# Performance work log

Hardware: AMD Instinct MI355X
Metric: run time of the kernel (lower is better)

## Reference

```python
import jax, jax.numpy as jnp
import numpy as np

DIM = 1024
NUM_HEADS = 16
HEAD_DIM = DIM // NUM_HEADS  # 64
LATENT = 128
Q_RANK = 256
B, S = 4, 2048


def setup_inputs() -> dict:
    key = jax.random.key(0)
    ks = jax.random.split(key, 12)
    w = lambda k, shape: jax.random.normal(k, shape, dtype=jnp.float32) * 0.02
    x = jax.random.normal(ks[0], (B, S, DIM), dtype=jnp.float32)
    mask = jnp.tril(jnp.ones((S, S), dtype=jnp.int32))[None, None, :, :]  # causal [1,1,S,S]
    return {
        "x": x,
        "mask": mask,
        "w_kvc": w(ks[1], (DIM, LATENT)),   "b_kvc": jnp.zeros((LATENT,), jnp.float32),
        "w_kvu": w(ks[2], (LATENT, 2 * DIM)), "b_kvu": jnp.zeros((2 * DIM,), jnp.float32),
        "w_qc":  w(ks[3], (DIM, Q_RANK)),   "b_qc": jnp.zeros((Q_RANK,), jnp.float32),
        "w_qu":  w(ks[4], (Q_RANK, DIM)),   "b_qu": jnp.zeros((DIM,), jnp.float32),
        "w_o":   w(ks[5], (DIM, DIM)),      "b_o": jnp.zeros((DIM,), jnp.float32),
    }


def reference(x, mask, w_kvc, b_kvc, w_kvu, b_kvu, w_qc, b_qc, w_qu, b_qu, w_o, b_o):
    b, s, _ = x.shape
    # low-rank KV path
    kv_latent = x @ w_kvc + b_kvc                      # [B,S,latent]
    kv_up = kv_latent @ w_kvu + b_kvu                  # [B,S,2*dim]
    K, V = jnp.split(kv_up, 2, axis=-1)                # each [B,S,dim]
    # low-rank Q path
    Q = (x @ w_qc + b_qc) @ w_qu + b_qu                # [B,S,dim]

    def split_heads(t):  # [B,S,dim] -> [B,H,S,hd]
        return t.reshape(b, s, NUM_HEADS, HEAD_DIM).transpose(0, 2, 1, 3)

    Qh, Kh, Vh = split_heads(Q), split_heads(K), split_heads(V)
    scores = jnp.einsum("bhsd,bhtd->bhst", Qh, Kh) / np.sqrt(HEAD_DIM).astype(np.float32)
    scores = jnp.where(mask == 0, jnp.float32(-1e9), scores)
    attn = jax.nn.softmax(scores, axis=-1)
    ctx = jnp.einsum("bhst,bhtd->bhsd", attn, Vh)      # [B,H,S,hd]
    ctx = ctx.transpose(0, 2, 1, 3).reshape(b, s, DIM)
    return ctx @ w_o + b_o
```

## Files before the change

### kernel.cpp

```cpp
#include <hip/hip_runtime.h>

typedef __attribute__((ext_vector_type(8))) short short8;
typedef __attribute__((ext_vector_type(4))) float f32x4;

#define DIM 1024
#define NH 16
#define HD 64
#define LAT 128
#define QR 256
#define NCAT (LAT + QR)
#define BB 4
#define SS 2048
#define BS (BB * SS)

#define SCALE_LOG2E 0.18033688011112042f

__device__ __forceinline__ unsigned short f2b(float f) {
  unsigned int u = __builtin_bit_cast(unsigned int, f);
  u += 0x7FFFu + ((u >> 16) & 1u);
  return (unsigned short)(u >> 16);
}
__device__ __forceinline__ float b2f(unsigned short h) {
  unsigned int u = ((unsigned int)h) << 16;
  return __builtin_bit_cast(float, u);
}
__device__ __forceinline__ unsigned int pack_bf16_pair(float f0, float f1) {
  unsigned int u0 = __builtin_bit_cast(unsigned int, f0) + 0x8000u;
  unsigned int u1 = __builtin_bit_cast(unsigned int, f1) + 0x8000u;
  return __builtin_amdgcn_perm(u1, u0, 0x07060302u);
}
__device__ __forceinline__ void gll16(const unsigned short* g, unsigned short* l) {
  __builtin_amdgcn_global_load_lds(
      (const __attribute__((address_space(1))) unsigned int*)g,
      (__attribute__((address_space(3))) unsigned int*)l, 16, 0, 0);
}

__global__ __launch_bounds__(256) void cvt_x(const float* __restrict__ in,
                                             unsigned short* __restrict__ out, int n4) {
  int i = blockIdx.x * 256 + threadIdx.x;
  if (i >= n4) return;
  f32x4 v = ((const f32x4*)in)[i];
  ushort4 o;
  o.x = f2b(v[0]); o.y = f2b(v[1]); o.z = f2b(v[2]); o.w = f2b(v[3]);
  ((ushort4*)out)[i] = o;
}

__global__ __launch_bounds__(256) void prep_weights(
    const float* __restrict__ w_kvc, const float* __restrict__ w_qc,
    const float* __restrict__ w_kvu, const float* __restrict__ w_qu,
    const float* __restrict__ w_o, const float* __restrict__ b_kvc,
    const float* __restrict__ b_qc, unsigned short* __restrict__ wcatT,
    unsigned short* __restrict__ wkvuT, unsigned short* __restrict__ wquT,
    unsigned short* __restrict__ woT, float* __restrict__ bias_cat) {
  __shared__ unsigned short T[64 * 72];
  const int id = blockIdx.x;
  const int tid = threadIdx.x;
  if (id >= 480) {
    if (tid < LAT) bias_cat[tid] = b_kvc[tid];
    else bias_cat[tid] = b_qc[tid - LAT];
    if (tid < 128) bias_cat[tid + 256] = b_qc[tid + 128];
    return;
  }
  const float* in; unsigned short* out; int K, N, tile;
  if (id < 32)       { in = w_kvc; out = wcatT;                       K = DIM; N = LAT;     tile = id; }
  else if (id < 96)  { in = w_qc;  out = wcatT + (size_t)LAT * DIM;   K = DIM; N = QR;      tile = id - 32; }
  else if (id < 160) { in = w_kvu; out = wkvuT;                       K = LAT; N = 2 * DIM; tile = id - 96; }
  else if (id < 224) { in = w_qu;  out = wquT;                        K = QR;  N = DIM;     tile = id - 160; }
  else               { in = w_o;   out = woT;                         K = DIM; N = DIM;     tile = id - 224; }
  const int ktiles = K >> 6;
  const int k0 = (tile % ktiles) * 64, n0 = (tile / ktiles) * 64;
  {
    const int r = tid >> 2, cq = (tid & 3) * 16;
#pragma unroll
    for (int j = 0; j < 4; ++j) {
      f32x4 v = *(const f32x4*)(in + (size_t)(k0 + r) * N + n0 + cq + j * 4);
      ushort4 o;
      o.x = f2b(v[0]); o.y = f2b(v[1]); o.z = f2b(v[2]); o.w = f2b(v[3]);
      *(ushort4*)(T + r * 72 + cq + j * 4) = o;
    }
  }
  __syncthreads();
#pragma unroll
  for (int s = 0; s < 2; ++s) {
    int idx = tid + s * 256;
    int nr = idx >> 3, kg = (idx & 7) * 8;
    short8 o;
#pragma unroll
    for (int i = 0; i < 8; i++) o[i] = T[(kg + i) * 72 + nr];
    *(short8*)(out + (size_t)(n0 + nr) * K + k0 + kg) = o;
  }
}

__global__ __launch_bounds__(256, 4) void gemm_lds(const unsigned short* __restrict__ A,
                                                   const unsigned short* __restrict__ WT,
                                                   const float* __restrict__ bias,
                                                   float* __restrict__ outF,
                                                   unsigned short* __restrict__ outB,
                                                   unsigned short* __restrict__ vtOut,
                                                   int N, int K, int lda, int ldout,
                                                   float scale, int nblk) {
  __shared__ unsigned short gsm[17408];
  const int tid = threadIdx.x;
  const int wave = tid >> 6, lane = tid & 63;
  const int ln = lane & 15, quad = lane >> 4;
  const int chunk = nblk >> 3;
  const int sw = (blockIdx.x & 7) * chunk + (blockIdx.x >> 3);
  const int nwx = N >> 7;
  const int bx = sw % nwx, by = sw / nwx;
  const int m0 = by * 128, n0 = bx * 128;
  const int wm = (wave >> 1) * 64, wn = (wave & 1) * 64;

  const int srow = wave * 32 + (lane >> 2);
  const int scol = (lane & 3) * 8;
  const unsigned short* Ag = A + (size_t)(m0 + srow) * lda + scol;
  const unsigned short* Bg = WT + (size_t)(n0 + srow) * K + scol;

  f32x4 acc[4][4];
#pragma unroll
  for (int i = 0; i < 4; i++)
#pragma unroll
    for (int j = 0; j < 4; j++) acc[i][j] = (f32x4){0.f, 0.f, 0.f, 0.f};

#define STAGE(buf, kk)                                                        \
  {                                                                           \
    unsigned short* Al = gsm + (buf) * 4096 + wave * 1024;                    \
    unsigned short* Bl = gsm + 8192 + (buf) * 4096 + wave * 1024;             \
    gll16(Ag + (kk), Al);                                                     \
    gll16(Ag + (size_t)16 * lda + (kk), Al + 512);                            \
    gll16(Bg + (kk), Bl);                                                     \
    gll16(Bg + (size_t)16 * K + (kk), Bl + 512);                              \
  }

  STAGE(0, 0);
  __syncthreads();
  const int T = K >> 5;
  int cur = 0;
  for (int t = 0; t < T; ++t) {
    if (t + 1 < T) STAGE(cur ^ 1, (t + 1) * 32);
    const unsigned short* Ab = gsm + cur * 4096;
    const unsigned short* Bb = gsm + 8192 + cur * 4096;
    short8 af[4], bf[4];
#pragma unroll
    for (int i = 0; i < 4; i++) {
      af[i] = *(const short8*)(Ab + (wm + i * 16 + ln) * 32 + quad * 8);
      bf[i] = *(const short8*)(Bb + (wn + i * 16 + ln) * 32 + quad * 8);
    }
#pragma unroll
    for (int mi = 0; mi < 4; mi++)
#pragma unroll
      for (int ni = 0; ni < 4; ni++)
        acc[mi][ni] =
            __builtin_amdgcn_mfma_f32_16x16x32_bf16(af[mi], bf[ni], acc[mi][ni], 0, 0, 0);
    __syncthreads();
    cur ^= 1;
  }
#undef STAGE

  if (vtOut && n0 >= DIM) {
#pragma unroll
    for (int mi = 0; mi < 4; mi++) {
      const int s = wm + mi * 16 + quad * 4;
#pragma unroll
      for (int ni = 0; ni < 4; ni++) {
        const int d = wn + ni * 16 + ln;
        const float bv = bias[n0 + d];
#pragma unroll
        for (int r = 0; r < 4; r++)
          gsm[d * 136 + s + r] = f2b(acc[mi][ni][r] + bv);
      }
    }
    __syncthreads();
    const int d0 = n0 - DIM, bb = m0 >> 11, s0l = m0 & (SS - 1);
#pragma unroll
    for (int t = 0; t < 8; ++t) {
      int idx = tid + t * 256;
      int dr = idx >> 4, cs = (idx & 15) * 8;
      short8 v = *(const short8*)(gsm + dr * 136 + cs);
      *(short8*)(vtOut + (size_t)(bb * DIM + d0 + dr) * SS + s0l + cs) = v;
    }
    return;
  }

#pragma unroll
  for (int mi = 0; mi < 4; mi++) {
    const int row = m0 + wm + mi * 16 + quad * 4;
#pragma unroll
    for (int ni = 0; ni < 4; ni++) {
      const int col = n0 + wn + ni * 16 + ln;
      const float bv = bias[col];
#pragma unroll
      for (int r = 0; r < 4; r++) {
        float v = (acc[mi][ni][r] + bv) * scale;
        size_t o = (size_t)(row + r) * ldout + col;
        if (outF) outF[o] = v;
        if (outB) outB[o] = f2b(v);
      }
    }
  }
}

__global__ __launch_bounds__(256, 4) void attn_mfma(const unsigned short* __restrict__ Qb,
                                                    const unsigned short* __restrict__ KVb,
                                                    const unsigned short* __restrict__ VTb,
                                                    unsigned short* __restrict__ ctxB) {
  __shared__ unsigned short smem[12288];
  unsigned short* Ks = smem;
  unsigned short* Vts = smem + 4096;
  unsigned short* Ps = smem + 8192;
  const int tid = threadIdx.x;
  const int wave = tid >> 6, lane = tid & 63;
  const int ln = lane & 15, quad = lane >> 4;
  const int hw = blockIdx.x;
  const int xcd = hw & 7, slot = hw >> 3;
  const int grp = xcd * 8 + (slot >> 4);
  const int pair = slot & 15;
  const int h = grp & 15, b = grp >> 4;
  const int tA = pair, tB = 31 - pair;
  const int s0A = tA * 64, s0B = tB * 64;
  const int ktmaxB = tB;
  const int qminA = s0A + wave * 16, qmaxA = qminA + 15;
  const int qminB = s0B + wave * 16, qmaxB = qminB + 15;

  short8 qfA[2], qfB[2];
  {
    const unsigned short* qa =
        Qb + (size_t)(b * SS + s0A + wave * 16 + ln) * DIM + h * HD + quad * 8;
    qfA[0] = *(const short8*)qa;
    qfA[1] = *(const short8*)(qa + 32);
    const unsigned short* qb2 =
        Qb + (size_t)(b * SS + s0B + wave * 16 + ln) * DIM + h * HD + quad * 8;
    qfB[0] = *(const short8*)qb2;
    qfB[1] = *(const short8*)(qb2 + 32);
  }

  f32x4 ocA[4], ocB[4];
  float lpA = 0.f, lpB = 0.f;
#pragma unroll
  for (int i = 0; i < 4; i++) {
    ocA[i] = (f32x4){0.f, 0.f, 0.f, 0.f};
    ocB[i] = (f32x4){0.f, 0.f, 0.f, 0.f};
  }

  unsigned short* Pw = Ps + wave * (16 * 64);
  const int swz = (ln & 7) << 3;

  const int srow = tid >> 3, sc8 = (tid & 7) * 8;
  const int ssc = sc8 ^ ((srow & 7) << 3);

  const unsigned short* kptr =
      KVb + (size_t)(b * SS + srow) * (2 * DIM) + h * HD + sc8;
  const unsigned short* vptr = VTb + (size_t)(b * DIM + h * HD + srow) * SS + sc8;
  const size_t kstep = (size_t)64 * 2 * DIM;
  const size_t krow32 = (size_t)32 * 2 * DIM;
  const size_t vrow32 = (size_t)32 * SS;

  short8 kreg0 = *(const short8*)kptr;
  short8 kreg1 = *(const short8*)(kptr + krow32);
  short8 vreg0 = *(const short8*)vptr;
  short8 vreg1 = *(const short8*)(vptr + vrow32);

  for (int kt = 0; kt <= ktmaxB; ++kt) {
    __syncthreads();
    *(short8*)(Ks + srow * 64 + ssc) = kreg0;
    *(short8*)(Ks + (srow + 32) * 64 + ssc) = kreg1;
    *(short8*)(Vts + srow * 64 + ssc) = vreg0;
    *(short8*)(Vts + (srow + 32) * 64 + ssc) = vreg1;
    __syncthreads();
    if (kt < ktmaxB) {
      kptr += kstep; vptr += 64;
      kreg0 = *(const short8*)kptr;
      kreg1 = *(const short8*)(kptr + krow32);
      vreg0 = *(const short8*)vptr;
      vreg1 = *(const short8*)(vptr + vrow32);
    }

    const int k0g = kt * 64;

    auto stream = [&](const short8* qf, f32x4* oc, float& lp, const int qminw,
                      const int qmaxw) {
      if (k0g > qmaxw) return;
      const bool needmask = (k0g + 63 > qminw);

      f32x4 sacc[4];
#pragma unroll
      for (int nt = 0; nt < 4; nt++) sacc[nt] = (f32x4){0.f, 0.f, 0.f, 0.f};
      __builtin_amdgcn_s_setprio(1);
#pragma unroll
      for (int kc = 0; kc < 2; kc++) {
        const int rc = (kc * 32 + quad * 8) ^ swz;
#pragma unroll
        for (int nt = 0; nt < 4; nt++) {
          if (k0g + nt * 16 > qmaxw) continue;
          short8 kfrag = *(const short8*)(Ks + (nt * 16 + ln) * 64 + rc);
          sacc[nt] =
              __builtin_amdgcn_mfma_f32_16x16x32_bf16(kfrag, qf[kc], sacc[nt], 0, 0, 0);
        }
      }
      __builtin_amdgcn_s_setprio(0);

      const int qg = qminw + ln;
      float lt = 0.f;
      if (!needmask) {
#pragma unroll
        for (int nt = 0; nt < 4; nt++) {
          float p0 = __builtin_exp2f(sacc[nt][0]);
          float p1 = __builtin_exp2f(sacc[nt][1]);
          float p2 = __builtin_exp2f(sacc[nt][2]);
          float p3 = __builtin_exp2f(sacc[nt][3]);
          uint2 pw;
          pw.x = pack_bf16_pair(p0, p1);
          pw.y = pack_bf16_pair(p2, p3);
          *(uint2*)(Pw + ln * 64 + ((nt * 16 + quad * 4) ^ swz)) = pw;
          lt += (p0 + p1) + (p2 + p3);
        }
      } else {
#pragma unroll
        for (int nt = 0; nt < 4; nt++) {
          const int base = k0g + nt * 16 + quad * 4;
          float pe[4];
#pragma unroll
          for (int r = 0; r < 4; r++) {
            float p = __builtin_exp2f(sacc[nt][r]);
            if (base + r > qg) p = 0.f;
            pe[r] = p;
          }
          uint2 pw;
          pw.x = pack_bf16_pair(pe[0], pe[1]);
          pw.y = pack_bf16_pair(pe[2], pe[3]);
          *(uint2*)(Pw + ln * 64 + ((nt * 16 + quad * 4) ^ swz)) = pw;
          lt += (pe[0] + pe[1]) + (pe[2] + pe[3]);
        }
      }
      lp += lt;

      __builtin_amdgcn_s_setprio(1);
#pragma unroll
      for (int kc = 0; kc < 2; kc++) {
        if (k0g + kc * 32 > qmaxw) continue;
        const int rc = (kc * 32 + quad * 8) ^ swz;
        short8 pfrag = *(const short8*)(Pw + ln * 64 + rc);
#pragma unroll
        for (int dt = 0; dt < 4; dt++) {
          short8 vfrag = *(const short8*)(Vts + (dt * 16 + ln) * 64 + rc);
          oc[dt] =
              __builtin_amdgcn_mfma_f32_16x16x32_bf16(pfrag, vfrag, oc[dt], 0, 0, 0);
        }
      }
      __builtin_amdgcn_s_setprio(0);
    };

    stream(qfA, ocA, lpA, qminA, qmaxA);
    stream(qfB, ocB, lpB, qminB, qmaxB);
  }

  lpA += __shfl_xor(lpA, 16, 64);
  lpA += __shfl_xor(lpA, 32, 64);
  lpB += __shfl_xor(lpB, 16, 64);
  lpB += __shfl_xor(lpB, 32, 64);
  float liA[4], liB[4];
#pragma unroll
  for (int r = 0; r < 4; r++) {
    liA[r] = 1.f / __shfl(lpA, quad * 4 + r, 64);
    liB[r] = 1.f / __shfl(lpB, quad * 4 + r, 64);
  }

  __syncthreads();
#pragma unroll
  for (int r = 0; r < 4; r++) {
#pragma unroll
    for (int dt = 0; dt < 4; dt++)
      smem[(wave * 16 + quad * 4 + r) * 72 + dt * 16 + ln] = f2b(ocA[dt][r] * liA[r]);
  }
  __syncthreads();
#pragma unroll
  for (int t = 0; t < 2; ++t) {
    int idx = tid + t * 256;
    int row = idx >> 3, c = idx & 7;
    short8 v = *(const short8*)(smem + row * 72 + c * 8);
    *(short8*)(ctxB + (size_t)(b * SS + s0A + row) * DIM + h * HD + c * 8) = v;
  }
  __syncthreads();
#pragma unroll
  for (int r = 0; r < 4; r++) {
#pragma unroll
    for (int dt = 0; dt < 4; dt++)
      smem[(wave * 16 + quad * 4 + r) * 72 + dt * 16 + ln] = f2b(ocB[dt][r] * liB[r]);
  }
  __syncthreads();
#pragma unroll
  for (int t = 0; t < 2; ++t) {
    int idx = tid + t * 256;
    int row = idx >> 3, c = idx & 7;
    short8 v = *(const short8*)(smem + row * 72 + c * 8);
    *(short8*)(ctxB + (size_t)(b * SS + s0B + row) * DIM + h * HD + c * 8) = v;
  }
}

extern "C" void kernel_launch(void* const* d_in, const int* in_sizes, int n_in,
                              void* d_out, int out_size, void* d_ws, size_t ws_size,
                              hipStream_t stream) {
  const float* x     = (const float*)d_in[0];
  const float* w_kvc = (const float*)d_in[2];
  const float* b_kvc = (const float*)d_in[3];
  const float* w_kvu = (const float*)d_in[4];
  const float* b_kvu = (const float*)d_in[5];
  const float* w_qc  = (const float*)d_in[6];
  const float* b_qc  = (const float*)d_in[7];
  const float* w_qu  = (const float*)d_in[8];
  const float* b_qu  = (const float*)d_in[9];
  const float* w_o   = (const float*)d_in[10];
  const float* b_o   = (const float*)d_in[11];
  float* out = (float*)d_out;

  unsigned short* xb     = (unsigned short*)d_ws;
  unsigned short* wcatT  = xb + (size_t)BS * DIM;
  unsigned short* wkvuT  = wcatT + (size_t)NCAT * DIM;
  unsigned short* wquT   = wkvuT + (size_t)LAT * 2 * DIM;
  unsigned short* woT    = wquT + (size_t)QR * DIM;
  unsigned short* kvqlat = woT + (size_t)DIM * DIM;
  unsigned short* kvup   = kvqlat + (size_t)BS * NCAT;
  unsigned short* Qbuf   = kvup + (size_t)BS * 2 * DIM;
  unsigned short* ctx    = Qbuf + (size_t)BS * DIM;
  float* bias_cat        = (float*)(ctx + (size_t)BS * DIM);

  cvt_x<<<(BS * DIM / 4 + 255) / 256, 256, 0, stream>>>(x, xb, BS * DIM / 4);
  prep_weights<<<481, 256, 0, stream>>>(w_kvc, w_qc, w_kvu, w_qu, w_o, b_kvc, b_qc,
                                        wcatT, wkvuT, wquT, woT, bias_cat);

  gemm_lds<<<dim3(BS / 128 * (NCAT / 128)), 256, 0, stream>>>(
      xb, wcatT, bias_cat, nullptr, kvqlat, nullptr, NCAT, DIM, DIM, NCAT, 1.0f,
      BS / 128 * (NCAT / 128));
  unsigned short* VT = xb;
  gemm_lds<<<dim3(BS / 128 * (2 * DIM / 128)), 256, 0, stream>>>(
      kvqlat, wkvuT, b_kvu, nullptr, kvup, VT, 2 * DIM, LAT, NCAT, 2 * DIM, 1.0f,
      BS / 128 * (2 * DIM / 128));
  gemm_lds<<<dim3(BS / 128 * (DIM / 128)), 256, 0, stream>>>(
      kvqlat + LAT, wquT, b_qu, nullptr, Qbuf, nullptr, DIM, QR, NCAT, DIM, SCALE_LOG2E,
      BS / 128 * (DIM / 128));
  attn_mfma<<<dim3(32 * NH * BB / 2), 256, 0, stream>>>(Qbuf, kvup, VT, ctx);
  gemm_lds<<<dim3(BS / 128 * (DIM / 128)), 256, 0, stream>>>(
      ctx, woT, b_o, out, nullptr, nullptr, DIM, DIM, DIM, DIM, 1.0f,
      BS / 128 * (DIM / 128));
}
```

Measured before the change: 254.8 us.

## Fuse prep kernels and up-projection GEMMs; shrink GEMM tile and swizzle LDS

Merges the x conversion and weight preparation into one launch, and merges the KV and Q up-projection GEMMs into a single launch that dispatches by block index. The GEMM tile shrinks from 128x128 to 64x128, doubling the block count, and LDS reads and writes use an XOR swizzle to cut bank conflicts. The aim is fewer kernel launches, better occupancy and wave balance on small-K GEMMs, and fewer LDS conflicts, at the cost of lower per-block data reuse and more B-tile reloads.

```diff
diff --git a/kernel.cpp b/kernel.cpp
--- a/kernel.cpp
+++ b/kernel.cpp
@@ -35,17 +35,8 @@
       (__attribute__((address_space(3))) unsigned int*)l, 16, 0, 0);
 }
 
-__global__ __launch_bounds__(256) void cvt_x(const float* __restrict__ in,
-                                             unsigned short* __restrict__ out, int n4) {
-  int i = blockIdx.x * 256 + threadIdx.x;
-  if (i >= n4) return;
-  f32x4 v = ((const f32x4*)in)[i];
-  ushort4 o;
-  o.x = f2b(v[0]); o.y = f2b(v[1]); o.z = f2b(v[2]); o.w = f2b(v[3]);
-  ((ushort4*)out)[i] = o;
-}
-
-__global__ __launch_bounds__(256) void prep_weights(
+__global__ __launch_bounds__(256) void cvt_prep(
+    const float* __restrict__ x, unsigned short* __restrict__ xb,
     const float* __restrict__ w_kvc, const float* __restrict__ w_qc,
     const float* __restrict__ w_kvu, const float* __restrict__ w_qu,
     const float* __restrict__ w_o, const float* __restrict__ b_kvc,
@@ -53,8 +44,16 @@
     unsigned short* __restrict__ wkvuT, unsigned short* __restrict__ wquT,
     unsigned short* __restrict__ woT, float* __restrict__ bias_cat) {
   __shared__ unsigned short T[64 * 72];
-  const int id = blockIdx.x;
   const int tid = threadIdx.x;
+  if (blockIdx.x < 8192) {
+    int i = blockIdx.x * 256 + tid;
+    f32x4 v = ((const f32x4*)x)[i];
+    ushort4 o;
+    o.x = f2b(v[0]); o.y = f2b(v[1]); o.z = f2b(v[2]); o.w = f2b(v[3]);
+    ((ushort4*)xb)[i] = o;
+    return;
+  }
+  const int id = blockIdx.x - 8192;
   if (id >= 480) {
     if (tid < LAT) bias_cat[tid] = b_kvc[tid];
     else bias_cat[tid] = b_qc[tid - LAT];
@@ -91,6 +90,112 @@
   }
 }
 
+__device__ __forceinline__ void gemm_body(
+    const unsigned short* __restrict__ A, const unsigned short* __restrict__ WT,
+    const float* __restrict__ bias, float* __restrict__ outF,
+    unsigned short* __restrict__ outB, unsigned short* __restrict__ vtOut,
+    int N, int K, int lda, int ldout, float scale, int nblk, int bid,
+    unsigned short* gsm) {
+  const int tid = threadIdx.x;
+  const int wave = tid >> 6, lane = tid & 63;
+  const int ln = lane & 15, quad = lane >> 4;
+  const int chunk = nblk >> 3;
+  const int sw = (bid & 7) * chunk + (bid >> 3);
+  const int nwx = N >> 7;
+  const int bx = sw % nwx, by = sw / nwx;
+  const int m0 = by * 64, n0 = bx * 128;
+  const int wm = (wave >> 1) * 32, wn = (wave & 1) * 64;
+
+  const int sr = lane >> 2;
+  const int scg = (lane & 3) ^ (sr & 3);
+  const unsigned short* Ag = A + (size_t)(m0 + wave * 16 + sr) * lda + scg * 8;
+  const unsigned short* Bg = WT + (size_t)(n0 + wave * 32 + sr) * K + scg * 8;
+
+  f32x4 acc[2][4];
+#pragma unroll
+  for (int i = 0; i < 2; i++)
+#pragma unroll
+    for (int j = 0; j < 4; j++) acc[i][j] = (f32x4){0.f, 0.f, 0.f, 0.f};
+
+#define STAGE(buf, kk)                                                        \
+  {                                                                           \
+    unsigned short* Al = gsm + (buf) * 2048 + wave * 512;                     \
+    unsigned short* Bl = gsm + 4096 + (buf) * 4096 + wave * 1024;             \
+    gll16(Ag + (kk), Al);                                                     \
+    gll16(Bg + (kk), Bl);                                                     \
+    gll16(Bg + (size_t)16 * K + (kk), Bl + 512);                              \
+  }
+
+  const int T = K >> 5;
+  STAGE(0, 0);
+  __syncthreads();
+  int cur = 0;
+  const int rc = (quad ^ (ln & 3)) * 8;
+  for (int t = 0; t < T; ++t) {
+    if (t + 1 < T) STAGE(cur ^ 1, (t + 1) * 32);
+    const unsigned short* Ab = gsm + cur * 2048;
+    const unsigned short* Bb = gsm + 4096 + cur * 4096;
+    short8 af[2], bf[4];
+#pragma unroll
+    for (int i = 0; i < 2; i++)
+      af[i] = *(const short8*)(Ab + (wm + i * 16 + ln) * 32 + rc);
+#pragma unroll
+    for (int i = 0; i < 4; i++)
+      bf[i] = *(const short8*)(Bb + (wn + i * 16 + ln) * 32 + rc);
+#pragma unroll
+    for (int mi = 0; mi < 2; mi++)
+#pragma unroll
+      for (int ni = 0; ni < 4; ni++)
+        acc[mi][ni] =
+            __builtin_amdgcn_mfma_f32_16x16x32_bf16(af[mi], bf[ni], acc[mi][ni], 0, 0, 0);
+    __syncthreads();
+    cur ^= 1;
+  }
+#undef STAGE
+
+  if (vtOut && n0 >= DIM) {
+#pragma unroll
+    for (int mi = 0; mi < 2; mi++) {
+      const int s = wm + mi * 16 + quad * 4;
+#pragma unroll
+      for (int ni = 0; ni < 4; ni++) {
+        const int d = wn + ni * 16 + ln;
+        const float bv = bias[n0 + d];
+#pragma unroll
+        for (int r = 0; r < 4; r++)
+          gsm[d * 72 + s + r] = f2b(acc[mi][ni][r] + bv);
+      }
+    }
+    __syncthreads();
+    const int d0 = n0 - DIM, bb = m0 >> 11, s0l = m0 & (SS - 1);
+#pragma unroll
+    for (int t = 0; t < 4; ++t) {
+      int idx = tid + t * 256;
+      int dr = idx >> 3, cs = (idx & 7) * 8;
+      short8 v = *(const short8*)(gsm + dr * 72 + cs);
+      *(short8*)(vtOut + (size_t)(bb * DIM + d0 + dr) * SS + s0l + cs) = v;
+    }
+    return;
+  }
+
+#pragma unroll
+  for (int mi = 0; mi < 2; mi++) {
+    const int row = m0 + wm + mi * 16 + quad * 4;
+#pragma unroll
+    for (int ni = 0; ni < 4; ni++) {
+      const int col = n0 + wn + ni * 16 + ln;
+      const float bv = bias[col];
+#pragma unroll
+      for (int r = 0; r < 4; r++) {
+        float v = (acc[mi][ni][r] + bv) * scale;
+        size_t o = (size_t)(row + r) * ldout + col;
+        if (outF) outF[o] = v;
+        if (outB) outB[o] = f2b(v);
+      }
+    }
+  }
+}
+
 __global__ __launch_bounds__(256, 4) void gemm_lds(const unsigned short* __restrict__ A,
                                                    const unsigned short* __restrict__ WT,
                                                    const float* __restrict__ bias,
@@ -100,103 +205,22 @@
                                                    int N, int K, int lda, int ldout,
                                                    float scale, int nblk) {
   __shared__ unsigned short gsm[17408];
-  const int tid = threadIdx.x;
-  const int wave = tid >> 6, lane = tid & 63;
-  const int ln = lane & 15, quad = lane >> 4;
-  const int chunk = nblk >> 3;
-  const int sw = (blockIdx.x & 7) * chunk + (blockIdx.x >> 3);
-  const int nwx = N >> 7;
-  const int bx = sw % nwx, by = sw / nwx;
-  const int m0 = by * 128, n0 = bx * 128;
-  const int wm = (wave >> 1) * 64, wn = (wave & 1) * 64;
-
-  const int srow = wave * 32 + (lane >> 2);
-  const int scol = (lane & 3) * 8;
-  const unsigned short* Ag = A + (size_t)(m0 + srow) * lda + scol;
-  const unsigned short* Bg = WT + (size_t)(n0 + srow) * K + scol;
-
-  f32x4 acc[4][4];
-#pragma unroll
-  for (int i = 0; i < 4; i++)
-#pragma unroll
-    for (int j = 0; j < 4; j++) acc[i][j] = (f32x4){0.f, 0.f, 0.f, 0.f};
-
-#define STAGE(buf, kk)                                                        \
-  {                                                                           \
-    unsigned short* Al = gsm + (buf) * 4096 + wave * 1024;                    \
-    unsigned short* Bl = gsm + 8192 + (buf) * 4096 + wave * 1024;             \
-    gll16(Ag + (kk), Al);                                                     \
-    gll16(Ag + (size_t)16 * lda + (kk), Al + 512);                            \
-    gll16(Bg + (kk), Bl);                                                     \
-    gll16(Bg + (size_t)16 * K + (kk), Bl + 512);                              \
-  }
-
-  STAGE(0, 0);
-  __syncthreads();
-  const int T = K >> 5;
-  int cur = 0;
-  for (int t = 0; t < T; ++t) {
-    if (t + 1 < T) STAGE(cur ^ 1, (t + 1) * 32);
-    const unsigned short* Ab = gsm + cur * 4096;
-    const unsigned short* Bb = gsm + 8192 + cur * 4096;
-    short8 af[4], bf[4];
-#pragma unroll
-    for (int i = 0; i < 4; i++) {
-      af[i] = *(const short8*)(Ab + (wm + i * 16 + ln) * 32 + quad * 8);
-      bf[i] = *(const short8*)(Bb + (wn + i * 16 + ln) * 32 + quad * 8);
-    }
-#pragma unroll
-    for (int mi = 0; mi < 4; mi++)
-#pragma unroll
-      for (int ni = 0; ni < 4; ni++)
-        acc[mi][ni] =
-            __builtin_amdgcn_mfma_f32_16x16x32_bf16(af[mi], bf[ni], acc[mi][ni], 0, 0, 0);
-    __syncthreads();
-    cur ^= 1;
-  }
-#undef STAGE
-
-  if (vtOut && n0 >= DIM) {
-#pragma unroll
-    for (int mi = 0; mi < 4; mi++) {
-      const int s = wm + mi * 16 + quad * 4;
-#pragma unroll
-      for (int ni = 0; ni < 4; ni++) {
-        const int d = wn + ni * 16 + ln;
-        const float bv = bias[n0 + d];
-#pragma unroll
-        for (int r = 0; r < 4; r++)
-          gsm[d * 136 + s + r] = f2b(acc[mi][ni][r] + bv);
-      }
-    }
-    __syncthreads();
-    const int d0 = n0 - DIM, bb = m0 >> 11, s0l = m0 & (SS - 1);
-#pragma unroll
-    for (int t = 0; t < 8; ++t) {
-      int idx = tid + t * 256;
-      int dr = idx >> 4, cs = (idx & 15) * 8;
-      short8 v = *(const short8*)(gsm + dr * 136 + cs);
-      *(short8*)(vtOut + (size_t)(bb * DIM + d0 + dr) * SS + s0l + cs) = v;
-    }
-    return;
-  }
-
-#pragma unroll
-  for (int mi = 0; mi < 4; mi++) {
-    const int row = m0 + wm + mi * 16 + quad * 4;
-#pragma unroll
-    for (int ni = 0; ni < 4; ni++) {
-      const int col = n0 + wn + ni * 16 + ln;
-      const float bv = bias[col];
-#pragma unroll
-      for (int r = 0; r < 4; r++) {
-        float v = (acc[mi][ni][r] + bv) * scale;
-        size_t o = (size_t)(row + r) * ldout + col;
-        if (outF) outF[o] = v;
-        if (outB) outB[o] = f2b(v);
-      }
-    }
-  }
+  gemm_body(A, WT, bias, outF, outB, vtOut, N, K, lda, ldout, scale, nblk,
+            blockIdx.x, gsm);
+}
+
+__global__ __launch_bounds__(256, 4) void gemm_s2q(
+    const unsigned short* __restrict__ kvqlat, const unsigned short* __restrict__ wkvuT,
+    const unsigned short* __restrict__ wquT, const float* __restrict__ b_kvu,
+    const float* __restrict__ b_qu, unsigned short* __restrict__ kvup,
+    unsigned short* __restrict__ VT, unsigned short* __restrict__ Qbuf) {
+  __shared__ unsigned short gsm[17408];
+  if (blockIdx.x < 2048)
+    gemm_body(kvqlat, wkvuT, b_kvu, nullptr, kvup, VT, 2 * DIM, LAT, NCAT,
+              2 * DIM, 1.0f, 2048, blockIdx.x, gsm);
+  else
+    gemm_body(kvqlat + LAT, wquT, b_qu, nullptr, Qbuf, nullptr, DIM, QR, NCAT,
+              DIM, SCALE_LOG2E, 1024, blockIdx.x - 2048, gsm);
 }
 
 __global__ __launch_bounds__(256, 4) void attn_mfma(const unsigned short* __restrict__ Qb,
@@ -423,22 +447,16 @@
   unsigned short* ctx    = Qbuf + (size_t)BS * DIM;
   float* bias_cat        = (float*)(ctx + (size_t)BS * DIM);
 
-  cvt_x<<<(BS * DIM / 4 + 255) / 256, 256, 0, stream>>>(x, xb, BS * DIM / 4);
-  prep_weights<<<481, 256, 0, stream>>>(w_kvc, w_qc, w_kvu, w_qu, w_o, b_kvc, b_qc,
-                                        wcatT, wkvuT, wquT, woT, bias_cat);
-
-  gemm_lds<<<dim3(BS / 128 * (NCAT / 128)), 256, 0, stream>>>(
-      xb, wcatT, bias_cat, nullptr, kvqlat, nullptr, NCAT, DIM, DIM, NCAT, 1.0f,
-      BS / 128 * (NCAT / 128));
+  cvt_prep<<<8673, 256, 0, stream>>>(x, xb, w_kvc, w_qc, w_kvu, w_qu, w_o,
+                                     b_kvc, b_qc, wcatT, wkvuT, wquT, woT,
+                                     bias_cat);
+
+  gemm_lds<<<384, 256, 0, stream>>>(xb, wcatT, bias_cat, nullptr, kvqlat,
+                                    nullptr, NCAT, DIM, DIM, NCAT, 1.0f, 384);
   unsigned short* VT = xb;
-  gemm_lds<<<dim3(BS / 128 * (2 * DIM / 128)), 256, 0, stream>>>(
-      kvqlat, wkvuT, b_kvu, nullptr, kvup, VT, 2 * DIM, LAT, NCAT, 2 * DIM, 1.0f,
-      BS / 128 * (2 * DIM / 128));
-  gemm_lds<<<dim3(BS / 128 * (DIM / 128)), 256, 0, stream>>>(
-      kvqlat + LAT, wquT, b_qu, nullptr, Qbuf, nullptr, DIM, QR, NCAT, DIM, SCALE_LOG2E,
-      BS / 128 * (DIM / 128));
-  attn_mfma<<<dim3(32 * NH * BB / 2), 256, 0, stream>>>(Qbuf, kvup, VT, ctx);
-  gemm_lds<<<dim3(BS / 128 * (DIM / 128)), 256, 0, stream>>>(
-      ctx, woT, b_o, out, nullptr, nullptr, DIM, DIM, DIM, DIM, 1.0f,
-      BS / 128 * (DIM / 128));
-}
+  gemm_s2q<<<3072, 256, 0, stream>>>(kvqlat, wkvuT, wquT, b_kvu, b_qu, kvup,
+                                     VT, Qbuf);
+  attn_mfma<<<1024, 256, 0, stream>>>(Qbuf, kvup, VT, ctx);
+  gemm_lds<<<1024, 256, 0, stream>>>(ctx, woT, b_o, out, nullptr, nullptr,
+                                     DIM, DIM, DIM, DIM, 1.0f, 1024);
+}
```

After: 250.2 us. Within noise of the previous version (-1.8%).
